# Optimization experiments

Measured on AMD Instinct MI355X. Metric: run time of the kernel, lower is better.

The kernel has to match this reference:

```python
import jax, jax.numpy as jnp
import numpy as np

N_EMBD = 2048
H_I = 16   # indexer heads
D_I = 32   # indexer dim


def setup_inputs() -> dict:
    key = jax.random.key(0)
    k1, k2, k3, k4 = jax.random.split(key, 4)
    x = jax.random.normal(k1, (2, 4096, N_EMBD), dtype=jnp.float32)
    # nn.Linear(in, out, bias=False) weights, stored (out, in) like torch
    s = 1.0 / np.sqrt(N_EMBD)
    Wq = jax.random.uniform(k2, (H_I * D_I, N_EMBD), jnp.float32, -s, s)
    Wk = jax.random.uniform(k3, (D_I, N_EMBD), jnp.float32, -s, s)
    Ww = jax.random.uniform(k4, (H_I, N_EMBD), jnp.float32, -s, s)
    return {"x": x, "Wq": Wq, "Wk": Wk, "Ww": Ww}


def reference(x, Wq, Wk, Ww):
    B, T, C = x.shape
    q = (x @ Wq.T).reshape(B, T, H_I, D_I)   # (B,T,H,D)
    k = x @ Wk.T                              # (B,T,D)
    w = x @ Ww.T                              # (B,T,H)
    scores = jnp.einsum('bqhd,bkd->bqhk', q, k)
    scores = jax.nn.relu(scores)
    importance = jnp.einsum('bqh,bqhk->bqk', w, scores)  # (B,T,T)
    return importance
```

## Files before the change

### kernel.cpp

```cpp
#include <hip/hip_runtime.h>
#include <hip/hip_bf16.h>
#include <stdint.h>


typedef __attribute__((ext_vector_type(8))) short bf16x8;
typedef __attribute__((ext_vector_type(4))) float f32x4;
typedef __attribute__((ext_vector_type(2))) __fp16 f16x2;

#define NPAD 640
#define KCOL 512
#define WCOL 544

__device__ __forceinline__ unsigned short f2bf(float f) {
  union { float f; unsigned u; } c; c.f = f;
  unsigned u = c.u;
  u += 0x7FFFu + ((u >> 16) & 1u);
  return (unsigned short)(u >> 16);
}

__device__ __forceinline__ f16x2 u32_to_h2(unsigned u) {
  union { unsigned u; f16x2 h; } c; c.u = u; return c.h;
}
__device__ __forceinline__ unsigned h2_to_u32(f16x2 h) {
  union { unsigned u; f16x2 h; } c; c.h = h; return c.u;
}

__device__ __forceinline__ void async_copy16(void* lds, const void* g) {
  __builtin_amdgcn_global_load_lds(
      (const __attribute__((address_space(1))) unsigned*)g,
      (__attribute__((address_space(3))) unsigned*)lds, 16, 0, 0);
}

__global__ __launch_bounds__(256) void pack_kernel(
    const float* __restrict__ x, const float* __restrict__ Wq,
    const float* __restrict__ Wk, const float* __restrict__ Ww,
    unsigned short* __restrict__ xb, unsigned short* __restrict__ Wp) {
  const int64_t NX4 = 16777216 / 4;
  int64_t i = (int64_t)blockIdx.x * 256 + threadIdx.x;
  if (i < NX4) {
    float4 v = ((const float4*)x)[i];
    ushort4 o;
    o.x = f2bf(v.x); o.y = f2bf(v.y); o.z = f2bf(v.z); o.w = f2bf(v.w);
    ((ushort4*)xb)[i] = o;
  } else {
    int p = (int)(i - NX4);
    int row = p >> 9;
    int col = (p & 511) << 2;
    float4 v = make_float4(0.f, 0.f, 0.f, 0.f);
    if (row < 512)      v = *(const float4*)(Wq + (int64_t)row * 2048 + col);
    else if (row < 544) v = *(const float4*)(Wk + (int64_t)(row - 512) * 2048 + col);
    else if (row < 560) v = *(const float4*)(Ww + (int64_t)(row - 544) * 2048 + col);
    ushort4 o;
    o.x = f2bf(v.x); o.y = f2bf(v.y); o.z = f2bf(v.z); o.w = f2bf(v.w);
    ((ushort4*)Wp)[p] = o;
  }
}

__global__ __launch_bounds__(256) void gemm_proj(
    const unsigned short* __restrict__ xb, const unsigned short* __restrict__ Wp,
    unsigned short* __restrict__ qkwb, float* __restrict__ wf) {
  __shared__ short lds_a[128 * 32];
  __shared__ short lds_b[128 * 32];
  const int tid = threadIdx.x;
  const int lane = tid & 63;
  const int l15 = lane & 15, quad = lane >> 4;
  const int wave = tid >> 6;
  const int wm = wave >> 1, wn = wave & 1;
  const int m0 = blockIdx.y * 128, n0 = blockIdx.x * 128;

  const int c0 = tid, c1 = tid + 256;
  const unsigned short* ga0 = xb + (int64_t)(m0 + (c0 >> 2)) * 2048 + (c0 & 3) * 8;
  const unsigned short* ga1 = xb + (int64_t)(m0 + (c1 >> 2)) * 2048 + (c1 & 3) * 8;
  const unsigned short* gb0 = Wp + (int64_t)(n0 + (c0 >> 2)) * 2048 + (c0 & 3) * 8;
  const unsigned short* gb1 = Wp + (int64_t)(n0 + (c1 >> 2)) * 2048 + (c1 & 3) * 8;

  f32x4 acc[4][4] = {};

  for (int kt = 0; kt < 64; ++kt) {
    const int ko = kt * 32;
    async_copy16(&lds_a[c0 * 8], ga0 + ko);
    async_copy16(&lds_a[c1 * 8], ga1 + ko);
    async_copy16(&lds_b[c0 * 8], gb0 + ko);
    async_copy16(&lds_b[c1 * 8], gb1 + ko);
    __syncthreads();
    bf16x8 af[4], bfr[4];
#pragma unroll
    for (int i = 0; i < 4; ++i)
      af[i] = *(const bf16x8*)&lds_a[(wm * 64 + i * 16 + l15) * 32 + quad * 8];
#pragma unroll
    for (int j = 0; j < 4; ++j)
      bfr[j] = *(const bf16x8*)&lds_b[(wn * 64 + j * 16 + l15) * 32 + quad * 8];
#pragma unroll
    for (int i = 0; i < 4; ++i)
#pragma unroll
      for (int j = 0; j < 4; ++j)
        acc[i][j] = __builtin_amdgcn_mfma_f32_16x16x32_bf16(af[i], bfr[j], acc[i][j], 0, 0, 0);
    __syncthreads();
  }

#pragma unroll
  for (int i = 0; i < 4; ++i)
#pragma unroll
    for (int j = 0; j < 4; ++j)
#pragma unroll
      for (int r = 0; r < 4; ++r) {
        int m = m0 + wm * 64 + i * 16 + quad * 4 + r;
        int n = n0 + wn * 64 + j * 16 + l15;
        float v = acc[i][j][r];
        qkwb[(int64_t)m * NPAD + n] = f2bf(v);
        if (n >= WCOL && n < WCOL + 16) wf[m * 16 + (n - WCOL)] = v;
      }
}

__global__ __launch_bounds__(256) void scores_kernel(
    const unsigned short* __restrict__ qkwb, const float* __restrict__ wf,
    float* __restrict__ out) {
  const int kt = blockIdx.x, qt = blockIdx.y, b = blockIdx.z;
  const int tid = threadIdx.x;
  const int lane = tid & 63;
  const int l15 = lane & 15, quad = lane >> 4;
  const int wave = tid >> 6;
  const int wk = wave & 1, wq = wave >> 1;

  __shared__ unsigned w2[8][132];

  const int qrow0 = b * 4096 + qt * 128;
  const int krow0 = b * 4096 + kt * 128;

  {
    const float4* ws = (const float4*)(wf + (int64_t)qrow0 * 16);
#pragma unroll
    for (int r = 0; r < 2; ++r) {
      int f = tid * 2 + r;
      float4 v = ws[f];
      int row = f >> 2, hb = (f & 3) * 4;
      f16x2 p01, p23;
      p01.x = (__fp16)v.x; p01.y = (__fp16)v.y;
      p23.x = (__fp16)v.z; p23.y = (__fp16)v.w;
      w2[(hb >> 1) + 0][row] = h2_to_u32(p01);
      w2[(hb >> 1) + 1][row] = h2_to_u32(p23);
    }
  }

  bf16x8 ka[4];
#pragma unroll
  for (int i = 0; i < 4; ++i) {
    int kk = krow0 + wk * 64 + i * 16 + l15;
    ka[i] = *(const bf16x8*)&qkwb[(int64_t)kk * NPAD + KCOL + quad * 8];
  }

  const unsigned short* qbase =
      qkwb + (int64_t)(qrow0 + wq * 64 + l15) * NPAD + quad * 8;

  f32x4 acc[4][4] = {};
  __syncthreads();

  const f16x2 hz = u32_to_h2(0u);
  const f32x4 z = {0.f, 0.f, 0.f, 0.f};

#pragma unroll
  for (int hp = 0; hp < 8; ++hp) {
    bf16x8 q0[4], q1[4];
#pragma unroll
    for (int j = 0; j < 4; ++j) {
      q0[j] = *(const bf16x8*)&qbase[(int64_t)j * 16 * NPAD + (2 * hp) * 32];
      q1[j] = *(const bf16x8*)&qbase[(int64_t)j * 16 * NPAD + (2 * hp + 1) * 32];
    }
    f16x2 wv[4];
#pragma unroll
    for (int j = 0; j < 4; ++j)
      wv[j] = u32_to_h2(w2[hp][wq * 64 + j * 16 + l15]);

#pragma unroll
    for (int i = 0; i < 4; ++i)
#pragma unroll
      for (int j = 0; j < 4; ++j) {
        f32x4 t0 = __builtin_amdgcn_mfma_f32_16x16x32_bf16(ka[i], q0[j], z, 0, 0, 0);
        f32x4 t1 = __builtin_amdgcn_mfma_f32_16x16x32_bf16(ka[i], q1[j], z, 0, 0, 0);
#pragma unroll
        for (int r = 0; r < 4; ++r) {
          f16x2 p = __builtin_amdgcn_cvt_pkrtz(t0[r], t1[r]);
          p = __builtin_elementwise_max(p, hz);
          acc[i][j][r] = __builtin_amdgcn_fdot2(p, wv[j], acc[i][j][r], false);
        }
      }
  }

#pragma unroll
  for (int i = 0; i < 4; ++i)
#pragma unroll
    for (int j = 0; j < 4; ++j) {
      int q = qt * 128 + wq * 64 + j * 16 + l15;
      int k = kt * 128 + wk * 64 + i * 16 + quad * 4;
      float4 v = make_float4(acc[i][j][0], acc[i][j][1], acc[i][j][2], acc[i][j][3]);
      *(float4*)&out[((int64_t)b * 4096 + q) * 4096 + k] = v;
    }
}

extern "C" void kernel_launch(void* const* d_in, const int* in_sizes, int n_in,
                              void* d_out, int out_size, void* d_ws, size_t ws_size,
                              hipStream_t stream) {
  const float* x  = (const float*)d_in[0];
  const float* Wq = (const float*)d_in[1];
  const float* Wk = (const float*)d_in[2];
  const float* Ww = (const float*)d_in[3];
  float* out = (float*)d_out;

  char* ws = (char*)d_ws;
  unsigned short* xb   = (unsigned short*)ws;
  unsigned short* Wp   = (unsigned short*)(ws + 33554432);
  unsigned short* qkwb = (unsigned short*)(ws + 36175872);
  float*          wf   = (float*)(ws + 46661632);

  pack_kernel<<<17664, 256, 0, stream>>>(x, Wq, Wk, Ww, xb, Wp);
  gemm_proj<<<dim3(5, 64), 256, 0, stream>>>(xb, Wp, qkwb, wf);
  scores_kernel<<<dim3(32, 32, 2), 256, 0, stream>>>(qkwb, wf, out);
}
```

Measured before the change: 311.2 us.

## Store Q head-major and K separately; shrink projection GEMM M-tile to 64

The projection GEMM now writes Q in a head-major layout (head, row, 32), K in its own dense (row, 32) buffer and w in fp32, replacing the single padded 640-wide row buffer. The scores kernel then reads each head's Q fragments from contiguous 64-byte rows instead of scattered 1280-byte-stride rows, which should improve cache-line use. The GEMM tile also drops from 128x128 to 64x128, doubling the grid to 640 blocks for better CU occupancy, at the cost of more B-tile reloads and less reuse per block.

New measurement: 284.9 us. -8.4%, faster.

```diff
diff --git a/kernel.cpp b/kernel.cpp
--- a/kernel.cpp
+++ b/kernel.cpp
@@ -6,10 +6,6 @@
 typedef __attribute__((ext_vector_type(8))) short bf16x8;
 typedef __attribute__((ext_vector_type(4))) float f32x4;
 typedef __attribute__((ext_vector_type(2))) __fp16 f16x2;
-
-#define NPAD 640
-#define KCOL 512
-#define WCOL 544
 
 __device__ __forceinline__ unsigned short f2bf(float f) {
   union { float f; unsigned u; } c; c.f = f;
@@ -58,42 +54,41 @@
 
 __global__ __launch_bounds__(256) void gemm_proj(
     const unsigned short* __restrict__ xb, const unsigned short* __restrict__ Wp,
-    unsigned short* __restrict__ qkwb, float* __restrict__ wf) {
-  __shared__ short lds_a[128 * 32];
+    unsigned short* __restrict__ qh, unsigned short* __restrict__ kh,
+    float* __restrict__ wf) {
+  __shared__ short lds_a[64 * 32];
   __shared__ short lds_b[128 * 32];
   const int tid = threadIdx.x;
   const int lane = tid & 63;
   const int l15 = lane & 15, quad = lane >> 4;
   const int wave = tid >> 6;
-  const int wm = wave >> 1, wn = wave & 1;
-  const int m0 = blockIdx.y * 128, n0 = blockIdx.x * 128;
+  const int wn = wave;
+  const int m0 = blockIdx.y * 64, n0 = blockIdx.x * 128;
 
   const int c0 = tid, c1 = tid + 256;
-  const unsigned short* ga0 = xb + (int64_t)(m0 + (c0 >> 2)) * 2048 + (c0 & 3) * 8;
-  const unsigned short* ga1 = xb + (int64_t)(m0 + (c1 >> 2)) * 2048 + (c1 & 3) * 8;
+  const unsigned short* ga  = xb + (int64_t)(m0 + (tid >> 2)) * 2048 + (tid & 3) * 8;
   const unsigned short* gb0 = Wp + (int64_t)(n0 + (c0 >> 2)) * 2048 + (c0 & 3) * 8;
   const unsigned short* gb1 = Wp + (int64_t)(n0 + (c1 >> 2)) * 2048 + (c1 & 3) * 8;
 
-  f32x4 acc[4][4] = {};
+  f32x4 acc[4][2] = {};
 
   for (int kt = 0; kt < 64; ++kt) {
     const int ko = kt * 32;
-    async_copy16(&lds_a[c0 * 8], ga0 + ko);
-    async_copy16(&lds_a[c1 * 8], ga1 + ko);
+    async_copy16(&lds_a[tid * 8], ga + ko);
     async_copy16(&lds_b[c0 * 8], gb0 + ko);
     async_copy16(&lds_b[c1 * 8], gb1 + ko);
     __syncthreads();
-    bf16x8 af[4], bfr[4];
+    bf16x8 af[4], bfr[2];
 #pragma unroll
     for (int i = 0; i < 4; ++i)
-      af[i] = *(const bf16x8*)&lds_a[(wm * 64 + i * 16 + l15) * 32 + quad * 8];
-#pragma unroll
-    for (int j = 0; j < 4; ++j)
-      bfr[j] = *(const bf16x8*)&lds_b[(wn * 64 + j * 16 + l15) * 32 + quad * 8];
+      af[i] = *(const bf16x8*)&lds_a[(i * 16 + l15) * 32 + quad * 8];
+#pragma unroll
+    for (int j = 0; j < 2; ++j)
+      bfr[j] = *(const bf16x8*)&lds_b[(wn * 32 + j * 16 + l15) * 32 + quad * 8];
 #pragma unroll
     for (int i = 0; i < 4; ++i)
 #pragma unroll
-      for (int j = 0; j < 4; ++j)
+      for (int j = 0; j < 2; ++j)
         acc[i][j] = __builtin_amdgcn_mfma_f32_16x16x32_bf16(af[i], bfr[j], acc[i][j], 0, 0, 0);
     __syncthreads();
   }
@@ -101,20 +96,21 @@
 #pragma unroll
   for (int i = 0; i < 4; ++i)
 #pragma unroll
-    for (int j = 0; j < 4; ++j)
+    for (int j = 0; j < 2; ++j)
 #pragma unroll
       for (int r = 0; r < 4; ++r) {
-        int m = m0 + wm * 64 + i * 16 + quad * 4 + r;
-        int n = n0 + wn * 64 + j * 16 + l15;
+        int m = m0 + i * 16 + quad * 4 + r;
+        int n = n0 + wn * 32 + j * 16 + l15;
         float v = acc[i][j][r];
-        qkwb[(int64_t)m * NPAD + n] = f2bf(v);
-        if (n >= WCOL && n < WCOL + 16) wf[m * 16 + (n - WCOL)] = v;
+        if (n < 512)      qh[((int64_t)(n >> 5) * 8192 + m) * 32 + (n & 31)] = f2bf(v);
+        else if (n < 544) kh[(int64_t)m * 32 + (n - 512)] = f2bf(v);
+        else if (n < 560) wf[m * 16 + (n - 544)] = v;
       }
 }
 
 __global__ __launch_bounds__(256) void scores_kernel(
-    const unsigned short* __restrict__ qkwb, const float* __restrict__ wf,
-    float* __restrict__ out) {
+    const unsigned short* __restrict__ qh, const unsigned short* __restrict__ kh,
+    const float* __restrict__ wf, float* __restrict__ out) {
   const int kt = blockIdx.x, qt = blockIdx.y, b = blockIdx.z;
   const int tid = threadIdx.x;
   const int lane = tid & 63;
@@ -146,11 +142,11 @@
 #pragma unroll
   for (int i = 0; i < 4; ++i) {
     int kk = krow0 + wk * 64 + i * 16 + l15;
-    ka[i] = *(const bf16x8*)&qkwb[(int64_t)kk * NPAD + KCOL + quad * 8];
+    ka[i] = *(const bf16x8*)&kh[(int64_t)kk * 32 + quad * 8];
   }
 
   const unsigned short* qbase =
-      qkwb + (int64_t)(qrow0 + wq * 64 + l15) * NPAD + quad * 8;
+      qh + (int64_t)(qrow0 + wq * 64 + l15) * 32 + quad * 8;
 
   f32x4 acc[4][4] = {};
   __syncthreads();
@@ -163,8 +159,8 @@
     bf16x8 q0[4], q1[4];
 #pragma unroll
     for (int j = 0; j < 4; ++j) {
-      q0[j] = *(const bf16x8*)&qbase[(int64_t)j * 16 * NPAD + (2 * hp) * 32];
-      q1[j] = *(const bf16x8*)&qbase[(int64_t)j * 16 * NPAD + (2 * hp + 1) * 32];
+      q0[j] = *(const bf16x8*)&qbase[(int64_t)(2 * hp) * 262144 + j * 512];
+      q1[j] = *(const bf16x8*)&qbase[(int64_t)(2 * hp + 1) * 262144 + j * 512];
     }
     f16x2 wv[4];
 #pragma unroll
@@ -207,12 +203,13 @@
   float* out = (float*)d_out;
 
   char* ws = (char*)d_ws;
-  unsigned short* xb   = (unsigned short*)ws;
-  unsigned short* Wp   = (unsigned short*)(ws + 33554432);
-  unsigned short* qkwb = (unsigned short*)(ws + 36175872);
-  float*          wf   = (float*)(ws + 46661632);
+  unsigned short* xb = (unsigned short*)ws;
+  unsigned short* Wp = (unsigned short*)(ws + 33554432);
+  unsigned short* qh = (unsigned short*)(ws + 36175872);
+  unsigned short* kh = (unsigned short*)(ws + 44564480);
+  float*          wf = (float*)(ws + 45088768);
 
   pack_kernel<<<17664, 256, 0, stream>>>(x, Wq, Wk, Ww, xb, Wp);
-  gemm_proj<<<dim3(5, 64), 256, 0, stream>>>(xb, Wp, qkwb, wf);
-  scores_kernel<<<dim3(32, 32, 2), 256, 0, stream>>>(qkwb, wf, out);
-}
+  gemm_proj<<<dim3(5, 128), 256, 0, stream>>>(xb, Wp, qh, kh, wf);
+  scores_kernel<<<dim3(32, 32, 2), 256, 0, stream>>>(qh, kh, wf, out);
+}
```
